# Performance work log

Measured on AMD Instinct MI355X. Metric: run time of the kernel, lower is better.

## Reference

```python
import jax, jax.numpy as jnp
from jax import lax
import numpy as np

B, T, H, IN = 64, 2048, 256, 1


def setup_inputs() -> dict:
    key = jax.random.key(0)
    ks = jax.random.split(key, 12)
    s = 1.0 / np.sqrt(H)  # torch LSTM init scale (use normal*s for simplicity)
    return {
        "x": jax.random.normal(ks[0], (B, T, IN), jnp.float32),
        "Wih0": jax.random.normal(ks[1], (4 * H, IN), jnp.float32) * s,
        "Whh0": jax.random.normal(ks[2], (4 * H, H), jnp.float32) * s,
        "bih0": jax.random.normal(ks[3], (4 * H,), jnp.float32) * s,
        "bhh0": jax.random.normal(ks[4], (4 * H,), jnp.float32) * s,
        "Wih1": jax.random.normal(ks[5], (4 * H, H), jnp.float32) * s,
        "Whh1": jax.random.normal(ks[6], (4 * H, H), jnp.float32) * s,
        "bih1": jax.random.normal(ks[7], (4 * H,), jnp.float32) * s,
        "bhh1": jax.random.normal(ks[8], (4 * H,), jnp.float32) * s,
        "fc_w": jax.random.normal(ks[9], (1, H), jnp.float32) * s,
        "fc_b": jax.random.normal(ks[10], (1,), jnp.float32) * s,
    }


def _lstm_layer(x, Wih, Whh, bih, bhh):
    # x: [B, T, D_in] -> h sequence [B, T, H]; torch gate order (i, f, g, o)
    Bb = x.shape[0]
    Hh = Whh.shape[1]
    # precompute input contribution for all timesteps: [B, T, 4H]
    xg = jnp.einsum('btd,gd->btg', x, Wih) + bih + bhh

    def step(carry, xt):
        h, c = carry
        g = xt + h @ Whh.T  # [B, 4H]
        i, f, gg, o = jnp.split(g, 4, axis=-1)
        i = jax.nn.sigmoid(i)
        f = jax.nn.sigmoid(f)
        gg = jnp.tanh(gg)
        o = jax.nn.sigmoid(o)
        c = f * c + i * gg
        h = o * jnp.tanh(c)
        return (h, c), h

    h0 = jnp.zeros((Bb, Hh), x.dtype)
    c0 = jnp.zeros((Bb, Hh), x.dtype)
    (_, _), hs = lax.scan(step, (h0, c0), jnp.swapaxes(xg, 0, 1))  # hs: [T, B, H]
    return jnp.swapaxes(hs, 0, 1)


def reference(x, Wih0, Whh0, bih0, bhh0, Wih1, Whh1, bih1, bhh1, fc_w, fc_b):
    h1 = _lstm_layer(x, Wih0, Whh0, bih0, bhh0)   # [B, T, H]
    h2 = _lstm_layer(h1, Wih1, Whh1, bih1, bhh1)  # [B, T, H]
    out = jnp.einsum('bth,oh->bto', h2, fc_w) + fc_b  # [B, T, 1]
    return out
```

## Files before the change

kernel.cpp:

```cpp
#include <hip/hip_runtime.h>

#define TT 2048
#define NTHR 512
#define NWG 128

#define ABORT_O  0
#define E0_O     128
#define E1P_O    256
#define GFL0A_O  512
#define GFL0B_O  2560
#define GFL1A_O  4608
#define GFL1B_O  6656
#define H0EXP_O  16384
#define H1R_O    278528
#define WS_TOTAL 409600

#define A0_HI   0
#define A0_LO   32768
#define A_IH_HI 0
#define A_IH_LO 32768
#define A_HH_HI 65536
#define A_HH_LO 98304
#define P_O     131072
#define CB_O    148480
#define BIAS_O  152576
#define FWL_O   152832
#define WIB_O   152896
#define XB_O    153152
#define SMEM_BYTES 153408

typedef __bf16 bf16;
typedef __bf16 bf16x8 __attribute__((ext_vector_type(8)));
typedef float f32x4 __attribute__((ext_vector_type(4)));
typedef unsigned int u32;
typedef u32 u32x4 __attribute__((ext_vector_type(4)));
typedef unsigned short u16;

__device__ __forceinline__ f32x4 MFMA(bf16x8 a, bf16x8 b, f32x4 c) {
  return __builtin_amdgcn_mfma_f32_16x16x32_bf16(a, b, c, 0, 0, 0);
}
__device__ __forceinline__ float sigf(float v) { return 1.0f / (1.0f + __expf(-v)); }
__device__ __forceinline__ u16 bfbits(float f) { return __builtin_bit_cast(u16, (bf16)f); }
__device__ __forceinline__ u32 pack2(float a, float b) {
  return ((u32)bfbits(b) << 16) | bfbits(a);
}

__device__ __forceinline__ bf16x8 ld16d(const void* p) {
  u32x4 v;
  asm volatile("global_load_dwordx4 %0, %1, off sc0 sc1" : "=v"(v) : "v"(p));
  return __builtin_bit_cast(bf16x8, v);
}
__device__ __forceinline__ void wait_all_loads() {
  asm volatile("s_waitcnt vmcnt(0)" ::: "memory");
  __builtin_amdgcn_sched_barrier(0);
}
__device__ __forceinline__ void drain_stores() {
  asm volatile("s_waitcnt vmcnt(0)" ::: "memory");
}
__device__ __forceinline__ void st32d(u32* p, u32 v) {
  asm volatile("global_store_dword %0, %1, off sc0 sc1" :: "v"(p), "v"(v) : "memory");
}
__device__ __forceinline__ void post_flag(u32* pA, u32* pB, u32 v) {
  asm volatile("global_store_dword %0, %1, off"         :: "v"(pA), "v"(v) : "memory");
  asm volatile("global_store_dword %0, %1, off sc0 sc1" :: "v"(pB), "v"(v) : "memory");
}
__device__ __forceinline__ void wait_ge(const u32* pA, const u32* pB, u32 need, u32* abortp) {
  int it = 0;
  for (;;) {
    u32 va, vb;
    asm volatile("global_load_dword %0, %1, off sc0\n\ts_waitcnt vmcnt(0)"
                 : "=v"(va) : "v"(pA) : "memory");
    asm volatile("global_load_dword %0, %1, off sc0 sc1\n\ts_waitcnt vmcnt(0)"
                 : "=v"(vb) : "v"(pB) : "memory");
    u32 v = va > vb ? va : vb;
    if (__all((int)(v >= need))) break;
    if (((++it) & 63) == 0) {
      u32 ab;
      asm volatile("global_load_dword %0, %1, off sc0 sc1\n\ts_waitcnt vmcnt(0)"
                   : "=v"(ab) : "v"(abortp) : "memory");
      if (__any((int)(ab != 0))) break;
      if (it >= (1 << 18)) {
        if (threadIdx.x == 0) st32d(abortp, 1u);
        break;
      }
    }
  }
}

extern "C" __global__ __launch_bounds__(NTHR, 2)
void lstm_persist(const float* __restrict__ x,
                  const float* __restrict__ Wih0, const float* __restrict__ Whh0,
                  const float* __restrict__ bih0, const float* __restrict__ bhh0,
                  const float* __restrict__ Wih1, const float* __restrict__ Whh1,
                  const float* __restrict__ bih1, const float* __restrict__ bhh1,
                  const float* __restrict__ fcw, const float* __restrict__ fcb,
                  float* __restrict__ out, char* __restrict__ ws)
{
  extern __shared__ char smem[];
  const int tid  = threadIdx.x;
  const int wg   = blockIdx.x;
  const int role = wg & 7;
  const int slot = wg >> 3;
  if (role > 1) return;

  u32* abortp = (u32*)(ws + ABORT_O);
  u32* e0     = (u32*)(ws + E0_O);
  u32* e1p    = (u32*)(ws + E1P_O);

  const int w = tid >> 6, l = tid & 63, lr = l & 15, lk = l >> 4;
  const int rowb = (w & 1) * 32, colb = (w >> 1) * 16;

  float* P    = (float*)(smem + P_O);
  float* cbuf = (float*)(smem + CB_O);
  float* bias = (float*)(smem + BIAS_O);

  if (role == 0) {
    bf16x8* Ahi = (bf16x8*)(smem + A0_HI);
    bf16x8* Alo = (bf16x8*)(smem + A0_LO);
    float* wib  = (float*)(smem + WIB_O);
    float* xb   = (float*)(smem + XB_O);

    for (int i = tid; i < 2048; i += NTHR) {
      int row = i >> 5, kb = i & 31;
      int grow = (row >> 4) * 256 + slot * 16 + (row & 15);
      const float* src = Whh0 + grow * 256 + kb * 8;
      bf16x8 hi, lo;
#pragma unroll
      for (int e = 0; e < 8; e++) { float v = src[e]; bf16 h = (bf16)v; hi[e] = h; lo[e] = (bf16)(v - (float)h); }
      Ahi[kb * 64 + row] = hi;  Alo[kb * 64 + row] = lo;
    }
    if (tid < 64) {
      int grow = (tid >> 4) * 256 + slot * 16 + (tid & 15);
      wib[tid]  = Wih0[grow];
      bias[tid] = bih0[grow] + bhh0[grow];
    }
    for (int i = tid; i < 1024; i += NTHR) cbuf[i] = 0.0f;
    __syncthreads();

    u32* gfA = (u32*)(ws + GFL0A_O);
    u32* gfB = (u32*)(ws + GFL0B_O);

    for (int s = 0; s <= TT; s++) {
      if (tid < 64) {
        const u32 *pA, *pB; u32 need;
        if (tid < 16)       { pA = gfA + tid * 32; pB = gfB + tid * 32; need = (u32)s; }
        else if (tid == 16) { pA = e1p; pB = e1p; need = (s >= 4 && s < TT) ? (u32)(s - 3) : 0u; }
        else                { pA = gfA; pB = gfB; need = 0u; }
        wait_ge(pA, pB, need, abortp);
        if (tid == 0 && slot == 0 && s > 0) st32d(e0, (u32)s);
      }
      if (s == TT) break;
      __syncthreads();

      const char* hp = ws + H0EXP_O + (size_t)((s - 1) & 3) * 65536;
      bf16x8 bh[8], bl[8];
#pragma unroll
      for (int ks = 0; ks < 8; ks++) {
        int kb = ks * 4 + lk;
        const char* p = hp + (size_t)(kb * 64 + colb + lr) * 16;
        bh[ks] = ld16d(p);
        bl[ks] = ld16d(p + 32768);
      }
      if (tid < 64) xb[tid] = x[tid * TT + s];
      wait_all_loads();

      f32x4 acc0 = {0.f,0.f,0.f,0.f}, acc1 = {0.f,0.f,0.f,0.f};
#pragma unroll
      for (int ks = 0; ks < 8; ks++) {
        int kb = ks * 4 + lk;
        bf16x8 a0h = Ahi[kb * 64 + rowb + lr], a1h = Ahi[kb * 64 + rowb + 16 + lr];
        bf16x8 a0l = Alo[kb * 64 + rowb + lr], a1l = Alo[kb * 64 + rowb + 16 + lr];
        acc0 = MFMA(a0h, bh[ks], acc0);  acc1 = MFMA(a1h, bh[ks], acc1);
        acc0 = MFMA(a0h, bl[ks], acc0);  acc1 = MFMA(a1h, bl[ks], acc1);
        acc0 = MFMA(a0l, bh[ks], acc0);  acc1 = MFMA(a1l, bh[ks], acc1);
      }
#pragma unroll
      for (int r = 0; r < 4; r++) {
        P[(rowb + lk * 4 + r) * 68 + colb + lr]      = acc0[r];
        P[(rowb + 16 + lk * 4 + r) * 68 + colb + lr] = acc1[r];
      }
      __syncthreads();

      {
        u32* eh = (u32*)(ws + H0EXP_O + (size_t)(s & 3) * 65536);
        u32* el = (u32*)((char*)eh + 32768 / 4 * 0 + 32768);
        int b = tid >> 3, p = tid & 7;
        float xv = xb[b];
        float hv[2], rv[2];
#pragma unroll
        for (int q = 0; q < 2; q++) {
          int d = p * 2 + q;
          float pi = P[(d) * 68 + b]      + wib[d] * xv      + bias[d];
          float pf = P[(16 + d) * 68 + b] + wib[16 + d] * xv + bias[16 + d];
          float pg = P[(32 + d) * 68 + b] + wib[32 + d] * xv + bias[32 + d];
          float po = P[(48 + d) * 68 + b] + wib[48 + d] * xv + bias[48 + d];
          float c = sigf(pf) * cbuf[d * 64 + b] + sigf(pi) * tanhf(pg);
          cbuf[d * 64 + b] = c;
          float h = sigf(po) * tanhf(c);
          hv[q] = h;  rv[q] = h - (float)((bf16)h);
        }
        int kbg = slot * 2 + (p >> 2);
        u32 wi = (u32)((kbg * 64 + b) * 4 + (p & 3));
        st32d(eh + wi, pack2(hv[0], hv[1]));
        st32d(el + wi, pack2(rv[0], rv[1]));
      }
      drain_stores();
      __syncthreads();
      if (tid == 0) post_flag(gfA + slot * 32, gfB + slot * 32, (u32)(s + 1));
    }
  } else {
    bf16x8* AihH = (bf16x8*)(smem + A_IH_HI);
    bf16x8* AihL = (bf16x8*)(smem + A_IH_LO);
    bf16x8* AhhH = (bf16x8*)(smem + A_HH_HI);
    bf16x8* AhhL = (bf16x8*)(smem + A_HH_LO);
    float* fwl   = (float*)(smem + FWL_O);

    for (int i = tid; i < 2048; i += NTHR) {
      int row = i >> 5, kb = i & 31;
      int grow = (row >> 4) * 256 + slot * 16 + (row & 15);
      {
        const float* src = Wih1 + grow * 256 + kb * 8;
        bf16x8 hi, lo;
#pragma unroll
        for (int e = 0; e < 8; e++) { float v = src[e]; bf16 h = (bf16)v; hi[e] = h; lo[e] = (bf16)(v - (float)h); }
        AihH[kb * 64 + row] = hi;  AihL[kb * 64 + row] = lo;
      }
      {
        const float* src = Whh1 + grow * 256 + kb * 8;
        bf16x8 hi, lo;
#pragma unroll
        for (int e = 0; e < 8; e++) { float v = src[e]; bf16 h = (bf16)v; hi[e] = h; lo[e] = (bf16)(v - (float)h); }
        AhhH[kb * 64 + row] = hi;  AhhL[kb * 64 + row] = lo;
      }
    }
    if (tid < 64) {
      int grow = (tid >> 4) * 256 + slot * 16 + (tid & 15);
      bias[tid] = bih1[grow] + bhh1[grow];
    }
    if (tid < 16) fwl[tid] = fcw[slot * 16 + tid];
    for (int i = tid; i < 1024; i += NTHR) cbuf[i] = 0.0f;
    __syncthreads();

    u32* gfA = (u32*)(ws + GFL1A_O);
    u32* gfB = (u32*)(ws + GFL1B_O);
    const float fb = fcb[0];

    for (int u = 0; u < TT; u++) {
      if (tid < 64) {
        const u32 *pA, *pB; u32 need;
        if (tid < 16)       { pA = gfA + tid * 32; pB = gfB + tid * 32; need = (u32)u; }
        else if (tid == 16) { pA = e0; pB = e0; need = (u32)(u + 1); }
        else                { pA = gfA; pB = gfB; need = 0u; }
        wait_ge(pA, pB, need, abortp);
        if (tid == 0 && slot == 0 && u > 0) st32d(e1p, (u32)u);
      }
      __syncthreads();

      const char* h0p = ws + H0EXP_O + (size_t)(u & 3) * 65536;
      const char* h1p = ws + H1R_O + (size_t)((u - 1) & 1) * 65536;
      bf16x8 b0h[8], b0l[8], b1h[8], b1l[8];
#pragma unroll
      for (int ks = 0; ks < 8; ks++) {
        int kb = ks * 4 + lk;
        const char* p0 = h0p + (size_t)(kb * 64 + colb + lr) * 16;
        const char* p1 = h1p + (size_t)(kb * 64 + colb + lr) * 16;
        b0h[ks] = ld16d(p0);  b0l[ks] = ld16d(p0 + 32768);
        b1h[ks] = ld16d(p1);  b1l[ks] = ld16d(p1 + 32768);
      }
      wait_all_loads();

      f32x4 acc0 = {0.f,0.f,0.f,0.f}, acc1 = {0.f,0.f,0.f,0.f};
#pragma unroll
      for (int ks = 0; ks < 8; ks++) {
        int kb = ks * 4 + lk;
        bf16x8 aih0 = AihH[kb * 64 + rowb + lr], aih1 = AihH[kb * 64 + rowb + 16 + lr];
        bf16x8 ail0 = AihL[kb * 64 + rowb + lr], ail1 = AihL[kb * 64 + rowb + 16 + lr];
        acc0 = MFMA(aih0, b0h[ks], acc0);  acc1 = MFMA(aih1, b0h[ks], acc1);
        acc0 = MFMA(aih0, b0l[ks], acc0);  acc1 = MFMA(aih1, b0l[ks], acc1);
        acc0 = MFMA(ail0, b0h[ks], acc0);  acc1 = MFMA(ail1, b0h[ks], acc1);
        bf16x8 ahh0 = AhhH[kb * 64 + rowb + lr], ahh1 = AhhH[kb * 64 + rowb + 16 + lr];
        bf16x8 ahl0 = AhhL[kb * 64 + rowb + lr], ahl1 = AhhL[kb * 64 + rowb + 16 + lr];
        acc0 = MFMA(ahh0, b1h[ks], acc0);  acc1 = MFMA(ahh1, b1h[ks], acc1);
        acc0 = MFMA(ahh0, b1l[ks], acc0);  acc1 = MFMA(ahh1, b1l[ks], acc1);
        acc0 = MFMA(ahl0, b1h[ks], acc0);  acc1 = MFMA(ahl1, b1h[ks], acc1);
      }
#pragma unroll
      for (int r = 0; r < 4; r++) {
        P[(rowb + lk * 4 + r) * 68 + colb + lr]      = acc0[r];
        P[(rowb + 16 + lk * 4 + r) * 68 + colb + lr] = acc1[r];
      }
      __syncthreads();

      {
        u32* rh = (u32*)(ws + H1R_O + (size_t)(u & 1) * 65536);
        u32* rl = (u32*)((char*)rh + 32768);
        int b = tid >> 3, p = tid & 7;
        float hv[2], rv[2];
#pragma unroll
        for (int q = 0; q < 2; q++) {
          int d = p * 2 + q;
          float pi = P[(d) * 68 + b]      + bias[d];
          float pf = P[(16 + d) * 68 + b] + bias[16 + d];
          float pg = P[(32 + d) * 68 + b] + bias[32 + d];
          float po = P[(48 + d) * 68 + b] + bias[48 + d];
          float c = sigf(pf) * cbuf[d * 64 + b] + sigf(pi) * tanhf(pg);
          cbuf[d * 64 + b] = c;
          float h = sigf(po) * tanhf(c);
          hv[q] = h;  rv[q] = h - (float)((bf16)h);
          P[d * 68 + b] = h;
        }
        int kbg = slot * 2 + (p >> 2);
        u32 wi = (u32)((kbg * 64 + b) * 4 + (p & 3));
        st32d(rh + wi, pack2(hv[0], hv[1]));
        st32d(rl + wi, pack2(rv[0], rv[1]));
      }
      drain_stores();
      __syncthreads();

      if (tid < 64) {
        float acc = 0.0f;
#pragma unroll
        for (int d = 0; d < 16; d++) acc += fwl[d] * P[d * 68 + tid];
        if (slot == 0) acc += fb;
        atomicAdd(out + (size_t)tid * TT + u, acc);
      }
      if (tid == 0) post_flag(gfA + slot * 32, gfB + slot * 32, (u32)(u + 1));
    }
  }
}

extern "C" void kernel_launch(void* const* d_in, const int* in_sizes, int n_in,
                              void* d_out, int out_size, void* d_ws, size_t ws_size,
                              hipStream_t stream) {
  (void)in_sizes; (void)n_in; (void)ws_size;
  hipFuncSetAttribute((const void*)lstm_persist,
                      hipFuncAttributeMaxDynamicSharedMemorySize, SMEM_BYTES);
  hipMemsetAsync(d_ws, 0, WS_TOTAL, stream);
  hipMemsetAsync(d_out, 0, (size_t)out_size * sizeof(float), stream);
  lstm_persist<<<dim3(NWG), dim3(NTHR), SMEM_BYTES, stream>>>(
      (const float*)d_in[0],
      (const float*)d_in[1], (const float*)d_in[2],
      (const float*)d_in[3], (const float*)d_in[4],
      (const float*)d_in[5], (const float*)d_in[6],
      (const float*)d_in[7], (const float*)d_in[8],
      (const float*)d_in[9], (const float*)d_in[10],
      (float*)d_out, (char*)d_ws);
}
```

Before: 10.91 ms.

## Unify both LSTM layers into one lockstep wavefront with a single global barrier

Replaces the two independently flagged layer pipelines with one global step barrier. At step t, 16 layer-0 workgroups compute h0[t] while 16 layer-1 workgroups compute h1[t-1], all 32 waiting on one shared flag array. A startup handshake checks whether all workgroups see each other through the local cache level, and if so uses lighter cache-scope loads and stores. The change also swaps tanhf for an exp-based tanh and moves the FC atomic after the flag post. This removes the separate per-layer flag waits and cross-layer counters, at the cost of a full 32-way barrier every step and reliance on the residency detection being correct.

```diff
diff --git a/kernel.cpp b/kernel.cpp
--- a/kernel.cpp
+++ b/kernel.cpp
@@ -2,18 +2,16 @@
 
 #define TT 2048
 #define NTHR 512
-#define NWG 128
-
-#define ABORT_O  0
-#define E0_O     128
-#define E1P_O    256
-#define GFL0A_O  512
-#define GFL0B_O  2560
-#define GFL1A_O  4608
-#define GFL1B_O  6656
-#define H0EXP_O  16384
-#define H1R_O    278528
-#define WS_TOTAL 409600
+#define NWG 256
+
+#define ABORT_O 0
+#define TOK_O   128
+#define VER_O   512
+#define FLA_O   1024
+#define FLB_O   5120
+#define H0_O    16384
+#define H1_O    147456
+#define WS_TOTAL 278528
 
 #define A0_HI   0
 #define A0_LO   32768
@@ -24,10 +22,10 @@
 #define P_O     131072
 #define CB_O    148480
 #define BIAS_O  152576
+#define WIB_O   152832
+#define XB_O    153088
 #define FWL_O   152832
-#define WIB_O   152896
-#define XB_O    153152
-#define SMEM_BYTES 153408
+#define SMEM_BYTES 153344
 
 typedef __bf16 bf16;
 typedef __bf16 bf16x8 __attribute__((ext_vector_type(8)));
@@ -40,54 +38,71 @@
   return __builtin_amdgcn_mfma_f32_16x16x32_bf16(a, b, c, 0, 0, 0);
 }
 __device__ __forceinline__ float sigf(float v) { return 1.0f / (1.0f + __expf(-v)); }
+__device__ __forceinline__ float tanhfast(float x) {
+  float e = __expf(2.0f * x);
+  return 1.0f - 2.0f / (e + 1.0f);
+}
 __device__ __forceinline__ u16 bfbits(float f) { return __builtin_bit_cast(u16, (bf16)f); }
 __device__ __forceinline__ u32 pack2(float a, float b) {
   return ((u32)bfbits(b) << 16) | bfbits(a);
 }
 
-__device__ __forceinline__ bf16x8 ld16d(const void* p) {
+__device__ __forceinline__ bf16x8 ld16x(const void* p, bool pure) {
   u32x4 v;
-  asm volatile("global_load_dwordx4 %0, %1, off sc0 sc1" : "=v"(v) : "v"(p));
+  if (pure) asm volatile("global_load_dwordx4 %0, %1, off sc0"     : "=v"(v) : "v"(p));
+  else      asm volatile("global_load_dwordx4 %0, %1, off sc0 sc1" : "=v"(v) : "v"(p));
   return __builtin_bit_cast(bf16x8, v);
 }
 __device__ __forceinline__ void wait_all_loads() {
   asm volatile("s_waitcnt vmcnt(0)" ::: "memory");
   __builtin_amdgcn_sched_barrier(0);
 }
-__device__ __forceinline__ void drain_stores() {
-  asm volatile("s_waitcnt vmcnt(0)" ::: "memory");
-}
-__device__ __forceinline__ void st32d(u32* p, u32 v) {
+__device__ __forceinline__ void st32x(u32* p, u32 v, bool pure) {
+  if (pure) asm volatile("global_store_dword %0, %1, off"          :: "v"(p), "v"(v) : "memory");
+  else      asm volatile("global_store_dword %0, %1, off sc0 sc1"  :: "v"(p), "v"(v) : "memory");
+}
+__device__ __forceinline__ void st32_deep(u32* p, u32 v) {
   asm volatile("global_store_dword %0, %1, off sc0 sc1" :: "v"(p), "v"(v) : "memory");
 }
-__device__ __forceinline__ void post_flag(u32* pA, u32* pB, u32 v) {
-  asm volatile("global_store_dword %0, %1, off"         :: "v"(pA), "v"(v) : "memory");
-  asm volatile("global_store_dword %0, %1, off sc0 sc1" :: "v"(pB), "v"(v) : "memory");
-}
-__device__ __forceinline__ void wait_ge(const u32* pA, const u32* pB, u32 need, u32* abortp) {
+__device__ __forceinline__ void st32_plain(u32* p, u32 v) {
+  asm volatile("global_store_dword %0, %1, off" :: "v"(p), "v"(v) : "memory");
+}
+__device__ __forceinline__ u32 ld_sc0(const u32* p) {
+  u32 v;
+  asm volatile("global_load_dword %0, %1, off sc0\n\ts_waitcnt vmcnt(0)"
+               : "=v"(v) : "v"(p) : "memory");
+  return v;
+}
+__device__ __forceinline__ u32 ld_deep(const u32* p) {
+  u32 v;
+  asm volatile("global_load_dword %0, %1, off sc0 sc1\n\ts_waitcnt vmcnt(0)"
+               : "=v"(v) : "v"(p) : "memory");
+  return v;
+}
+
+__device__ __forceinline__ void wait_flags(const u32* fA, const u32* fB, u32 need,
+                                           u32* abortp, bool pure) {
+  const int lane = threadIdx.x & 63;
+  const u32* pA = fA + (lane & 31) * 32;
+  const u32* pB = fB + (lane & 31) * 32;
   int it = 0;
   for (;;) {
-    u32 va, vb;
-    asm volatile("global_load_dword %0, %1, off sc0\n\ts_waitcnt vmcnt(0)"
-                 : "=v"(va) : "v"(pA) : "memory");
-    asm volatile("global_load_dword %0, %1, off sc0 sc1\n\ts_waitcnt vmcnt(0)"
-                 : "=v"(vb) : "v"(pB) : "memory");
-    u32 v = va > vb ? va : vb;
+    u32 v = pure ? ld_sc0(pA) : ld_deep(pB);
     if (__all((int)(v >= need))) break;
-    if (((++it) & 63) == 0) {
-      u32 ab;
-      asm volatile("global_load_dword %0, %1, off sc0 sc1\n\ts_waitcnt vmcnt(0)"
-                   : "=v"(ab) : "v"(abortp) : "memory");
+    ++it;
+    if (pure && (it & 31) == 0) {
+      u32 vb = ld_deep(pB);
+      if (__all((int)(vb >= need))) break;
+    }
+    if ((it & 127) == 0) {
+      u32 ab = ld_deep(abortp);
       if (__any((int)(ab != 0))) break;
-      if (it >= (1 << 18)) {
-        if (threadIdx.x == 0) st32d(abortp, 1u);
-        break;
-      }
+      if (it >= (1 << 17)) { if (lane == 0) st32_deep(abortp, 1u); break; }
     }
   }
 }
 
-extern "C" __global__ __launch_bounds__(NTHR, 2)
+extern "C" __global__ __launch_bounds__(NTHR)
 void lstm_persist(const float* __restrict__ x,
                   const float* __restrict__ Wih0, const float* __restrict__ Whh0,
                   const float* __restrict__ bih0, const float* __restrict__ bhh0,
@@ -97,15 +112,40 @@
                   float* __restrict__ out, char* __restrict__ ws)
 {
   extern __shared__ char smem[];
-  const int tid  = threadIdx.x;
-  const int wg   = blockIdx.x;
-  const int role = wg & 7;
+  const int tid = threadIdx.x;
+  const int wg  = blockIdx.x;
+  if (wg & 7) return;
   const int slot = wg >> 3;
-  if (role > 1) return;
+  const bool isL1 = slot >= 16;
+  const int sl = isL1 ? slot - 16 : slot;
 
   u32* abortp = (u32*)(ws + ABORT_O);
-  u32* e0     = (u32*)(ws + E0_O);
-  u32* e1p    = (u32*)(ws + E1P_O);
+  u32* tok    = (u32*)(ws + TOK_O);
+  u32* ver    = (u32*)(ws + VER_O);
+  u32* fA     = (u32*)(ws + FLA_O);
+  u32* fB     = (u32*)(ws + FLB_O);
+
+  __shared__ u32 pure_sh;
+  if (tid == 0) st32_plain(&tok[slot], 1u);
+  if (tid < 64) {
+    const u32* pp = tok + (tid & 31);
+    u32 myver = 0;
+    for (int it = 0; it < (1 << 15); ++it) {
+      u32 v = ld_sc0(pp);
+      if (__all((int)(v != 0))) { myver = 1; break; }
+    }
+    if (tid == 0) st32_deep(&ver[slot], myver + 1u);
+    const u32* vp = ver + (tid & 31);
+    u32 vv = 0;
+    for (int it = 0; it < (1 << 17); ++it) {
+      vv = ld_deep(vp);
+      if (__all((int)(vv != 0))) break;
+    }
+    int allpure = __all((int)(vv == 2u));
+    if (tid == 0) pure_sh = (u32)allpure;
+  }
+  __syncthreads();
+  const bool pure = (pure_sh != 0);
 
   const int w = tid >> 6, l = tid & 63, lr = l & 15, lk = l >> 4;
   const int rowb = (w & 1) * 32, colb = (w >> 1) * 16;
@@ -114,15 +154,13 @@
   float* cbuf = (float*)(smem + CB_O);
   float* bias = (float*)(smem + BIAS_O);
 
-  if (role == 0) {
+  if (!isL1) {
     bf16x8* Ahi = (bf16x8*)(smem + A0_HI);
     bf16x8* Alo = (bf16x8*)(smem + A0_LO);
     float* wib  = (float*)(smem + WIB_O);
-    float* xb   = (float*)(smem + XB_O);
-
     for (int i = tid; i < 2048; i += NTHR) {
       int row = i >> 5, kb = i & 31;
-      int grow = (row >> 4) * 256 + slot * 16 + (row & 15);
+      int grow = (row >> 4) * 256 + sl * 16 + (row & 15);
       const float* src = Whh0 + grow * 256 + kb * 8;
       bf16x8 hi, lo;
 #pragma unroll
@@ -130,83 +168,9 @@
       Ahi[kb * 64 + row] = hi;  Alo[kb * 64 + row] = lo;
     }
     if (tid < 64) {
-      int grow = (tid >> 4) * 256 + slot * 16 + (tid & 15);
+      int grow = (tid >> 4) * 256 + sl * 16 + (tid & 15);
       wib[tid]  = Wih0[grow];
       bias[tid] = bih0[grow] + bhh0[grow];
-    }
-    for (int i = tid; i < 1024; i += NTHR) cbuf[i] = 0.0f;
-    __syncthreads();
-
-    u32* gfA = (u32*)(ws + GFL0A_O);
-    u32* gfB = (u32*)(ws + GFL0B_O);
-
-    for (int s = 0; s <= TT; s++) {
-      if (tid < 64) {
-        const u32 *pA, *pB; u32 need;
-        if (tid < 16)       { pA = gfA + tid * 32; pB = gfB + tid * 32; need = (u32)s; }
-        else if (tid == 16) { pA = e1p; pB = e1p; need = (s >= 4 && s < TT) ? (u32)(s - 3) : 0u; }
-        else                { pA = gfA; pB = gfB; need = 0u; }
-        wait_ge(pA, pB, need, abortp);
-        if (tid == 0 && slot == 0 && s > 0) st32d(e0, (u32)s);
-      }
-      if (s == TT) break;
-      __syncthreads();
-
-      const char* hp = ws + H0EXP_O + (size_t)((s - 1) & 3) * 65536;
-      bf16x8 bh[8], bl[8];
-#pragma unroll
-      for (int ks = 0; ks < 8; ks++) {
-        int kb = ks * 4 + lk;
-        const char* p = hp + (size_t)(kb * 64 + colb + lr) * 16;
-        bh[ks] = ld16d(p);
-        bl[ks] = ld16d(p + 32768);
-      }
-      if (tid < 64) xb[tid] = x[tid * TT + s];
-      wait_all_loads();
-
-      f32x4 acc0 = {0.f,0.f,0.f,0.f}, acc1 = {0.f,0.f,0.f,0.f};
-#pragma unroll
-      for (int ks = 0; ks < 8; ks++) {
-        int kb = ks * 4 + lk;
-        bf16x8 a0h = Ahi[kb * 64 + rowb + lr], a1h = Ahi[kb * 64 + rowb + 16 + lr];
-        bf16x8 a0l = Alo[kb * 64 + rowb + lr], a1l = Alo[kb * 64 + rowb + 16 + lr];
-        acc0 = MFMA(a0h, bh[ks], acc0);  acc1 = MFMA(a1h, bh[ks], acc1);
-        acc0 = MFMA(a0h, bl[ks], acc0);  acc1 = MFMA(a1h, bl[ks], acc1);
-        acc0 = MFMA(a0l, bh[ks], acc0);  acc1 = MFMA(a1l, bh[ks], acc1);
-      }
-#pragma unroll
-      for (int r = 0; r < 4; r++) {
-        P[(rowb + lk * 4 + r) * 68 + colb + lr]      = acc0[r];
-        P[(rowb + 16 + lk * 4 + r) * 68 + colb + lr] = acc1[r];
-      }
-      __syncthreads();
-
-      {
-        u32* eh = (u32*)(ws + H0EXP_O + (size_t)(s & 3) * 65536);
-        u32* el = (u32*)((char*)eh + 32768 / 4 * 0 + 32768);
-        int b = tid >> 3, p = tid & 7;
-        float xv = xb[b];
-        float hv[2], rv[2];
-#pragma unroll
-        for (int q = 0; q < 2; q++) {
-          int d = p * 2 + q;
-          float pi = P[(d) * 68 + b]      + wib[d] * xv      + bias[d];
-          float pf = P[(16 + d) * 68 + b] + wib[16 + d] * xv + bias[16 + d];
-          float pg = P[(32 + d) * 68 + b] + wib[32 + d] * xv + bias[32 + d];
-          float po = P[(48 + d) * 68 + b] + wib[48 + d] * xv + bias[48 + d];
-          float c = sigf(pf) * cbuf[d * 64 + b] + sigf(pi) * tanhf(pg);
-          cbuf[d * 64 + b] = c;
-          float h = sigf(po) * tanhf(c);
-          hv[q] = h;  rv[q] = h - (float)((bf16)h);
-        }
-        int kbg = slot * 2 + (p >> 2);
-        u32 wi = (u32)((kbg * 64 + b) * 4 + (p & 3));
-        st32d(eh + wi, pack2(hv[0], hv[1]));
-        st32d(el + wi, pack2(rv[0], rv[1]));
-      }
-      drain_stores();
-      __syncthreads();
-      if (tid == 0) post_flag(gfA + slot * 32, gfB + slot * 32, (u32)(s + 1));
     }
   } else {
     bf16x8* AihH = (bf16x8*)(smem + A_IH_HI);
@@ -214,10 +178,9 @@
     bf16x8* AhhH = (bf16x8*)(smem + A_HH_HI);
     bf16x8* AhhL = (bf16x8*)(smem + A_HH_LO);
     float* fwl   = (float*)(smem + FWL_O);
-
     for (int i = tid; i < 2048; i += NTHR) {
       int row = i >> 5, kb = i & 31;
-      int grow = (row >> 4) * 256 + slot * 16 + (row & 15);
+      int grow = (row >> 4) * 256 + sl * 16 + (row & 15);
       {
         const float* src = Wih1 + grow * 256 + kb * 8;
         bf16x8 hi, lo;
@@ -234,97 +197,161 @@
       }
     }
     if (tid < 64) {
-      int grow = (tid >> 4) * 256 + slot * 16 + (tid & 15);
+      int grow = (tid >> 4) * 256 + sl * 16 + (tid & 15);
       bias[tid] = bih1[grow] + bhh1[grow];
     }
-    if (tid < 16) fwl[tid] = fcw[slot * 16 + tid];
-    for (int i = tid; i < 1024; i += NTHR) cbuf[i] = 0.0f;
+    if (tid < 16) fwl[tid] = fcw[sl * 16 + tid];
+  }
+  for (int i = tid; i < 1024; i += NTHR) cbuf[i] = 0.0f;
+  __syncthreads();
+
+  const float fb = fcb[0];
+
+  for (int t = 0; t <= TT; ++t) {
+    if (t > 0) {
+      if (tid < 64) wait_flags(fA, fB, (u32)t, abortp, pure);
+      __syncthreads();
+    }
+
+    if (!isL1) {
+      if (t < TT) {
+        float* wib = (float*)(smem + WIB_O);
+        float* xb  = (float*)(smem + XB_O);
+        const char* hp = ws + H0_O + (size_t)((t - 1) & 1) * 65536;
+        bf16x8 bh[8], bl[8];
+#pragma unroll
+        for (int ks = 0; ks < 8; ks++) {
+          int kb = ks * 4 + lk;
+          const char* p = hp + (size_t)(kb * 64 + colb + lr) * 16;
+          bh[ks] = ld16x(p, pure);
+          bl[ks] = ld16x(p + 32768, pure);
+        }
+        if (tid < 64) xb[tid] = x[(size_t)tid * TT + t];
+        wait_all_loads();
+
+        bf16x8* Ahi = (bf16x8*)(smem + A0_HI);
+        bf16x8* Alo = (bf16x8*)(smem + A0_LO);
+        f32x4 acc0 = {0.f,0.f,0.f,0.f}, acc1 = {0.f,0.f,0.f,0.f};
+#pragma unroll
+        for (int ks = 0; ks < 8; ks++) {
+          int kb = ks * 4 + lk;
+          bf16x8 a0h = Ahi[kb * 64 + rowb + lr], a1h = Ahi[kb * 64 + rowb + 16 + lr];
+          bf16x8 a0l = Alo[kb * 64 + rowb + lr], a1l = Alo[kb * 64 + rowb + 16 + lr];
+          acc0 = MFMA(a0h, bh[ks], acc0);  acc1 = MFMA(a1h, bh[ks], acc1);
+          acc0 = MFMA(a0h, bl[ks], acc0);  acc1 = MFMA(a1h, bl[ks], acc1);
+          acc0 = MFMA(a0l, bh[ks], acc0);  acc1 = MFMA(a1l, bh[ks], acc1);
+        }
+#pragma unroll
+        for (int r = 0; r < 4; r++) {
+          P[(rowb + lk * 4 + r) * 68 + colb + lr]      = acc0[r];
+          P[(rowb + 16 + lk * 4 + r) * 68 + colb + lr] = acc1[r];
+        }
+        __syncthreads();
+
+        {
+          u32* eh = (u32*)(ws + H0_O + (size_t)(t & 1) * 65536);
+          u32* el = (u32*)((char*)eh + 32768);
+          int b = tid >> 3, p = tid & 7;
+          float xv = xb[b];
+          float hv[2], rv[2];
+#pragma unroll
+          for (int q = 0; q < 2; q++) {
+            int d = p * 2 + q;
+            float pi = P[(d) * 68 + b]      + wib[d] * xv      + bias[d];
+            float pf = P[(16 + d) * 68 + b] + wib[16 + d] * xv + bias[16 + d];
+            float pg = P[(32 + d) * 68 + b] + wib[32 + d] * xv + bias[32 + d];
+            float po = P[(48 + d) * 68 + b] + wib[48 + d] * xv + bias[48 + d];
+            float c = sigf(pf) * cbuf[d * 64 + b] + sigf(pi) * tanhfast(pg);
+            cbuf[d * 64 + b] = c;
+            float h = sigf(po) * tanhfast(c);
+            hv[q] = h;  rv[q] = h - (float)((bf16)h);
+          }
+          int kbg = sl * 2 + (p >> 2);
+          u32 wi = (u32)((kbg * 64 + b) * 4 + (p & 3));
+          st32x(eh + wi, pack2(hv[0], hv[1]), pure);
+          st32x(el + wi, pack2(rv[0], rv[1]), pure);
+        }
+      }
+    } else {
+      if (t >= 1) {
+        const char* h0p = ws + H0_O + (size_t)((t - 1) & 1) * 65536;
+        const char* h1p = ws + H1_O + (size_t)(t & 1) * 65536;
+        bf16x8 b0h[8], b0l[8], b1h[8], b1l[8];
+#pragma unroll
+        for (int ks = 0; ks < 8; ks++) {
+          int kb = ks * 4 + lk;
+          const char* p0 = h0p + (size_t)(kb * 64 + colb + lr) * 16;
+          const char* p1 = h1p + (size_t)(kb * 64 + colb + lr) * 16;
+          b0h[ks] = ld16x(p0, pure);  b0l[ks] = ld16x(p0 + 32768, pure);
+          b1h[ks] = ld16x(p1, pure);  b1l[ks] = ld16x(p1 + 32768, pure);
+        }
+        wait_all_loads();
+
+        bf16x8* AihH = (bf16x8*)(smem + A_IH_HI);
+        bf16x8* AihL = (bf16x8*)(smem + A_IH_LO);
+        bf16x8* AhhH = (bf16x8*)(smem + A_HH_HI);
+        bf16x8* AhhL = (bf16x8*)(smem + A_HH_LO);
+        f32x4 acc0 = {0.f,0.f,0.f,0.f}, acc1 = {0.f,0.f,0.f,0.f};
+#pragma unroll
+        for (int ks = 0; ks < 8; ks++) {
+          int kb = ks * 4 + lk;
+          bf16x8 aih0 = AihH[kb * 64 + rowb + lr], aih1 = AihH[kb * 64 + rowb + 16 + lr];
+          bf16x8 ail0 = AihL[kb * 64 + rowb + lr], ail1 = AihL[kb * 64 + rowb + 16 + lr];
+          acc0 = MFMA(aih0, b0h[ks], acc0);  acc1 = MFMA(aih1, b0h[ks], acc1);
+          acc0 = MFMA(aih0, b0l[ks], acc0);  acc1 = MFMA(aih1, b0l[ks], acc1);
+          acc0 = MFMA(ail0, b0h[ks], acc0);  acc1 = MFMA(ail1, b0h[ks], acc1);
+          bf16x8 ahh0 = AhhH[kb * 64 + rowb + lr], ahh1 = AhhH[kb * 64 + rowb + 16 + lr];
+          bf16x8 ahl0 = AhhL[kb * 64 + rowb + lr], ahl1 = AhhL[kb * 64 + rowb + 16 + lr];
+          acc0 = MFMA(ahh0, b1h[ks], acc0);  acc1 = MFMA(ahh1, b1h[ks], acc1);
+          acc0 = MFMA(ahh0, b1l[ks], acc0);  acc1 = MFMA(ahh1, b1l[ks], acc1);
+          acc0 = MFMA(ahl0, b1h[ks], acc0);  acc1 = MFMA(ahl1, b1h[ks], acc1);
+        }
+#pragma unroll
+        for (int r = 0; r < 4; r++) {
+          P[(rowb + lk * 4 + r) * 68 + colb + lr]      = acc0[r];
+          P[(rowb + 16 + lk * 4 + r) * 68 + colb + lr] = acc1[r];
+        }
+        __syncthreads();
+
+        {
+          u32* rh = (u32*)(ws + H1_O + (size_t)((t - 1) & 1) * 65536);
+          u32* rl = (u32*)((char*)rh + 32768);
+          int b = tid >> 3, p = tid & 7;
+          float hv[2], rv[2];
+#pragma unroll
+          for (int q = 0; q < 2; q++) {
+            int d = p * 2 + q;
+            float pi = P[(d) * 68 + b]      + bias[d];
+            float pf = P[(16 + d) * 68 + b] + bias[16 + d];
+            float pg = P[(32 + d) * 68 + b] + bias[32 + d];
+            float po = P[(48 + d) * 68 + b] + bias[48 + d];
+            float c = sigf(pf) * cbuf[d * 64 + b] + sigf(pi) * tanhfast(pg);
+            cbuf[d * 64 + b] = c;
+            float h = sigf(po) * tanhfast(c);
+            hv[q] = h;  rv[q] = h - (float)((bf16)h);
+            P[d * 68 + b] = h;
+          }
+          int kbg = sl * 2 + (p >> 2);
+          u32 wi = (u32)((kbg * 64 + b) * 4 + (p & 3));
+          st32x(rh + wi, pack2(hv[0], hv[1]), pure);
+          st32x(rl + wi, pack2(rv[0], rv[1]), pure);
+        }
+      }
+    }
+
+    asm volatile("s_waitcnt vmcnt(0)" ::: "memory");
     __syncthreads();
-
-    u32* gfA = (u32*)(ws + GFL1A_O);
-    u32* gfB = (u32*)(ws + GFL1B_O);
-    const float fb = fcb[0];
-
-    for (int u = 0; u < TT; u++) {
-      if (tid < 64) {
-        const u32 *pA, *pB; u32 need;
-        if (tid < 16)       { pA = gfA + tid * 32; pB = gfB + tid * 32; need = (u32)u; }
-        else if (tid == 16) { pA = e0; pB = e0; need = (u32)(u + 1); }
-        else                { pA = gfA; pB = gfB; need = 0u; }
-        wait_ge(pA, pB, need, abortp);
-        if (tid == 0 && slot == 0 && u > 0) st32d(e1p, (u32)u);
-      }
-      __syncthreads();
-
-      const char* h0p = ws + H0EXP_O + (size_t)(u & 3) * 65536;
-      const char* h1p = ws + H1R_O + (size_t)((u - 1) & 1) * 65536;
-      bf16x8 b0h[8], b0l[8], b1h[8], b1l[8];
-#pragma unroll
-      for (int ks = 0; ks < 8; ks++) {
-        int kb = ks * 4 + lk;
-        const char* p0 = h0p + (size_t)(kb * 64 + colb + lr) * 16;
-        const char* p1 = h1p + (size_t)(kb * 64 + colb + lr) * 16;
-        b0h[ks] = ld16d(p0);  b0l[ks] = ld16d(p0 + 32768);
-        b1h[ks] = ld16d(p1);  b1l[ks] = ld16d(p1 + 32768);
-      }
-      wait_all_loads();
-
-      f32x4 acc0 = {0.f,0.f,0.f,0.f}, acc1 = {0.f,0.f,0.f,0.f};
-#pragma unroll
-      for (int ks = 0; ks < 8; ks++) {
-        int kb = ks * 4 + lk;
-        bf16x8 aih0 = AihH[kb * 64 + rowb + lr], aih1 = AihH[kb * 64 + rowb + 16 + lr];
-        bf16x8 ail0 = AihL[kb * 64 + rowb + lr], ail1 = AihL[kb * 64 + rowb + 16 + lr];
-        acc0 = MFMA(aih0, b0h[ks], acc0);  acc1 = MFMA(aih1, b0h[ks], acc1);
-        acc0 = MFMA(aih0, b0l[ks], acc0);  acc1 = MFMA(aih1, b0l[ks], acc1);
-        acc0 = MFMA(ail0, b0h[ks], acc0);  acc1 = MFMA(ail1, b0h[ks], acc1);
-        bf16x8 ahh0 = AhhH[kb * 64 + rowb + lr], ahh1 = AhhH[kb * 64 + rowb + 16 + lr];
-        bf16x8 ahl0 = AhhL[kb * 64 + rowb + lr], ahl1 = AhhL[kb * 64 + rowb + 16 + lr];
-        acc0 = MFMA(ahh0, b1h[ks], acc0);  acc1 = MFMA(ahh1, b1h[ks], acc1);
-        acc0 = MFMA(ahh0, b1l[ks], acc0);  acc1 = MFMA(ahh1, b1l[ks], acc1);
-        acc0 = MFMA(ahl0, b1h[ks], acc0);  acc1 = MFMA(ahl1, b1h[ks], acc1);
-      }
-#pragma unroll
-      for (int r = 0; r < 4; r++) {
-        P[(rowb + lk * 4 + r) * 68 + colb + lr]      = acc0[r];
-        P[(rowb + 16 + lk * 4 + r) * 68 + colb + lr] = acc1[r];
-      }
-      __syncthreads();
-
-      {
-        u32* rh = (u32*)(ws + H1R_O + (size_t)(u & 1) * 65536);
-        u32* rl = (u32*)((char*)rh + 32768);
-        int b = tid >> 3, p = tid & 7;
-        float hv[2], rv[2];
-#pragma unroll
-        for (int q = 0; q < 2; q++) {
-          int d = p * 2 + q;
-          float pi = P[(d) * 68 + b]      + bias[d];
-          float pf = P[(16 + d) * 68 + b] + bias[16 + d];
-          float pg = P[(32 + d) * 68 + b] + bias[32 + d];
-          float po = P[(48 + d) * 68 + b] + bias[48 + d];
-          float c = sigf(pf) * cbuf[d * 64 + b] + sigf(pi) * tanhf(pg);
-          cbuf[d * 64 + b] = c;
-          float h = sigf(po) * tanhf(c);
-          hv[q] = h;  rv[q] = h - (float)((bf16)h);
-          P[d * 68 + b] = h;
-        }
-        int kbg = slot * 2 + (p >> 2);
-        u32 wi = (u32)((kbg * 64 + b) * 4 + (p & 3));
-        st32d(rh + wi, pack2(hv[0], hv[1]));
-        st32d(rl + wi, pack2(rv[0], rv[1]));
-      }
-      drain_stores();
-      __syncthreads();
-
-      if (tid < 64) {
-        float acc = 0.0f;
-#pragma unroll
-        for (int d = 0; d < 16; d++) acc += fwl[d] * P[d * 68 + tid];
-        if (slot == 0) acc += fb;
-        atomicAdd(out + (size_t)tid * TT + u, acc);
-      }
-      if (tid == 0) post_flag(gfA + slot * 32, gfB + slot * 32, (u32)(u + 1));
+    if (tid == 0 && t < TT) {
+      st32_plain(fA + slot * 32, (u32)(t + 1));
+      st32_deep (fB + slot * 32, (u32)(t + 1));
+    }
+    if (isL1 && t >= 1 && tid < 64) {
+      float* fwl = (float*)(smem + FWL_O);
+      float acc = 0.0f;
+#pragma unroll
+      for (int d = 0; d < 16; d++) acc += fwl[d] * P[d * 68 + tid];
+      if (sl == 0) acc += fb;
+      atomicAdd(out + (size_t)tid * TT + (t - 1), acc);
     }
   }
 }
```

Result: slower. 42.00 ms (+285.1%).
